# Performance work log

Hardware: AMD Instinct MI355X
Metric: run time of the kernel (lower is better)

The kernel has to match this reference:

```python
import jax, jax.numpy as jnp
import numpy as np
from jax import lax

B, T_ENC, T_DEC = 512, 64, 64
A = 64            # num_activities (pad token id = A)
ATTR_V = 10       # categorical attr vocab
ATTR_E, ACT_E, CF, ZD = 16, 64, 512, 128
TOT_ATTR = ATTR_E + 1           # 17
TDIM = TOT_ATTR // 2 + CF       # 8 + 512 = 520


def _lin(x, W, b):
    # torch nn.Linear: W is [out, in]
    return x @ W.T + b


def _cell(x, h, c, Wih, Whh, b):
    # torch LSTM cell, gate order i,f,g,o
    g = x @ Wih.T + h @ Whh.T + b
    i, f, gg, o = jnp.split(g, 4, axis=-1)
    c = jax.nn.sigmoid(f) * c + jax.nn.sigmoid(i) * jnp.tanh(gg)
    h = jax.nn.sigmoid(o) * jnp.tanh(c)
    return h, c


def setup_inputs() -> dict:
    key = jax.random.key(0)
    ks = iter(jax.random.split(key, 64))
    def n(shape, s=0.05):
        return jax.random.normal(next(ks), shape, jnp.float32) * s
    rng = np.random.default_rng(0)
    lens = rng.integers(2, T_ENC, size=B)
    acts_np = rng.integers(0, A - 1, size=(B, T_ENC))
    acts_np[np.arange(T_ENC)[None, :] >= lens[:, None]] = A  # pad token (max value -> argmax = len)
    return dict(
        attr_cat=jnp.asarray(rng.integers(0, ATTR_V, size=B), jnp.int32),
        attr_num=jax.random.uniform(next(ks), (B,), jnp.float32),
        acts=jnp.asarray(acts_np, jnp.int32),
        ts=jax.random.uniform(next(ks), (B, T_ENC), jnp.float32),
        epsilon=n((B, ZD), 1.0),
        attr_emb=n((ATTR_V, ATTR_E)),
        a2a_W=n((TOT_ATTR // 2, TOT_ATTR)), a2a_b=n((TOT_ATTR // 2,)),
        act_emb=n((A + 1, ACT_E)).at[A].set(0.0),  # padding_idx row zeroed
        eWih=n((4 * CF, ACT_E + 1)), eWhh=n((4 * CF, CF)), ebih=n((4 * CF,)), ebhh=n((4 * CF,)),
        mean_W=n((ZD, TDIM)), mean_b=n((ZD,)),
        var_W=n((ZD, TDIM)), var_b=n((ZD,)),
        z2t_W=n((TDIM, ZD)), z2t_b=n((TDIM,)),
        tc1_W=n((TDIM // 2, TDIM)), tc1_b=n((TDIM // 2,)),
        tc2_W=n((ATTR_V, TDIM // 2)), tc2_b=n((ATTR_V,)),
        tn1_W=n((TDIM // 2, TDIM)), tn1_b=n((TDIM // 2,)),
        tn2_W=n((1, TDIM // 2)), tn2_b=n((1,)),
        aWih=n((4 * CF, TDIM + ACT_E)), aWhh=n((4 * CF, CF)), abih=n((4 * CF,)), abhh=n((4 * CF,)),
        tWih=n((4 * CF, TDIM + ACT_E + 1)), tWhh=n((4 * CF, CF)), tbih=n((4 * CF,)), tbhh=n((4 * CF,)),
        e2act_W=n((A, CF)), e2act_b=n((A,)),
        ts1_W=n((CF // 2, CF)), ts1_b=n((CF // 2,)),
        ts2_W=n((1, CF // 2)), ts2_b=n((1,)),
    )


def reference(attr_cat, attr_num, acts, ts, epsilon,
              attr_emb, a2a_W, a2a_b, act_emb,
              eWih, eWhh, ebih, ebhh,
              mean_W, mean_b, var_W, var_b,
              z2t_W, z2t_b,
              tc1_W, tc1_b, tc2_W, tc2_b,
              tn1_W, tn1_b, tn2_W, tn2_b,
              aWih, aWhh, abih, abhh,
              tWih, tWhh, tbih, tbhh,
              e2act_W, e2act_b,
              ts1_W, ts1_b, ts2_W, ts2_b):
    # ---------- Encoder ----------
    e_attrs = jnp.concatenate([attr_emb[attr_cat], attr_num[:, None]], axis=1)   # [B,17]
    e_attrs = jax.nn.relu(_lin(e_attrs, a2a_W, a2a_b))                            # [B,8]
    x = jnp.concatenate([act_emb[acts], ts[:, :, None]], axis=2)                  # [B,T,ACT_E+1]
    eb = ebih + ebhh
    def enc_step(carry, xt):
        h, c = carry
        h, c = _cell(xt, h, c, eWih, eWhh, eb)
        return (h, c), h
    h0 = jnp.zeros((x.shape[0], CF), x.dtype)
    _, hs = lax.scan(enc_step, (h0, h0), jnp.swapaxes(x, 0, 1))
    cf_all = jnp.swapaxes(hs, 0, 1)                                               # [B,T,CF]
    # packed-sequence equivalence: LSTM is causal, we only read step lens-1
    lens = jnp.argmax(acts, axis=1)
    cf = cf_all[jnp.arange(cf_all.shape[0]), lens - 1]                            # [B,CF]
    t = jnp.concatenate([e_attrs, cf], axis=1)                                    # [B,TDIM]
    mean = _lin(t, mean_W, mean_b)
    var = _lin(t, var_W, var_b)
    z = mean + var * epsilon                                                      # reparameterization
    # ---------- Decoder ----------
    t_rec = jax.nn.relu(_lin(z, z2t_W, z2t_b))                                    # [B,TDIM]
    attr_cat_rec = jax.nn.softmax(_lin(jax.nn.relu(_lin(t_rec, tc1_W, tc1_b)), tc2_W, tc2_b), axis=1)
    attr_num_rec = jax.nn.sigmoid(_lin(jax.nn.relu(_lin(t_rec, tn1_W, tn1_b)), tn2_W, tn2_b))
    Bsz = t_rec.shape[0]
    ab, tb = abih + abhh, tbih + tbhh
    eot = jnp.broadcast_to(act_emb[A - 1], (Bsz, ACT_E))
    carry0 = (h0, h0, h0, h0, eot, jnp.zeros((Bsz, 1), t_rec.dtype))
    def dec_step(carry, _):
        h_a, c_a, h_t, c_t, ae, tsc = carry
        h_a, c_a = _cell(jnp.concatenate([t_rec, ae], 1), h_a, c_a, aWih, aWhh, ab)
        logits = _lin(h_a, e2act_W, e2act_b)                                      # [B,A]
        ae2 = act_emb[jnp.argmax(logits, axis=1)]                                 # greedy feedback
        h_t, c_t = _cell(jnp.concatenate([t_rec, ae2, tsc], 1), h_t, c_t, tWih, tWhh, tb)
        tsn = _lin(jax.nn.relu(_lin(h_t, ts1_W, ts1_b)), ts2_W, ts2_b)            # [B,1]
        return (h_a, c_a, h_t, c_t, ae2, tsn), (logits, tsn[:, 0])
    _, (logits_all, ts_all) = lax.scan(dec_step, carry0, None, length=T_DEC)
    acts_rec = jax.nn.softmax(jnp.swapaxes(logits_all, 0, 1), axis=2)             # [B,T_DEC,A]
    ts_rec = jnp.swapaxes(ts_all, 0, 1)                                           # [B,T_DEC]
    return (attr_cat_rec, attr_num_rec, acts_rec, ts_rec, mean, var)
```

## Files before the change

kernel.cpp:

```cpp
#include <hip/hip_runtime.h>
#include <math.h>


#define B 512
#define TT 64
#define CF 512
#define G4 2048
#define ZD 128
#define TDIM 520

typedef unsigned short u16;
typedef unsigned int u32;
typedef unsigned long long u64;
typedef short bf16x8 __attribute__((ext_vector_type(8)));
typedef float f32x4 __attribute__((ext_vector_type(4)));

__device__ __forceinline__ float sigm(float x) { return 1.f / (1.f + expf(-x)); }
__device__ __forceinline__ u16 f2bf(float f) {
    unsigned u = __float_as_uint(f);
    u += 0x7fffu + ((u >> 16) & 1u);
    return (u16)(u >> 16);
}
__device__ __forceinline__ float bf2f(u16 s) { return __uint_as_float(((unsigned)s) << 16); }
__device__ __forceinline__ u32 packbf(float v) {
    u16 hh = f2bf(v);
    u16 hl = f2bf(v - bf2f(hh));
    return (u32)hh | ((u32)hl << 16);
}

__device__ __forceinline__ void ast32(u32* p, u32 v) {
    __hip_atomic_store(p, v, __ATOMIC_RELAXED, __HIP_MEMORY_SCOPE_AGENT);
}
__device__ __forceinline__ u64 ald64(const u64* p) {
    return __hip_atomic_load(p, __ATOMIC_RELAXED, __HIP_MEMORY_SCOPE_AGENT);
}
__device__ __forceinline__ void astf(float* p, float v) {
    __hip_atomic_store(p, v, __ATOMIC_RELAXED, __HIP_MEMORY_SCOPE_AGENT);
}
__device__ __forceinline__ float aldf(const float* p) {
    return __hip_atomic_load(p, __ATOMIC_RELAXED, __HIP_MEMORY_SCOPE_AGENT);
}

__device__ __forceinline__ void unpk8(u64 a, u64 b, u64 c, u64 d,
                                      uint4& hi, uint4& lo) {
    u32 a0 = (u32)a, a1 = (u32)(a >> 32);
    u32 b0 = (u32)b, b1 = (u32)(b >> 32);
    u32 c0 = (u32)c, c1 = (u32)(c >> 32);
    u32 d0 = (u32)d, d1 = (u32)(d >> 32);
    hi.x = (a0 & 0xffffu) | (a1 << 16);  lo.x = (a0 >> 16) | (a1 & 0xffff0000u);
    hi.y = (b0 & 0xffffu) | (b1 << 16);  lo.y = (b0 >> 16) | (b1 & 0xffff0000u);
    hi.z = (c0 & 0xffffu) | (c1 << 16);  lo.z = (c0 >> 16) | (c1 & 0xffff0000u);
    hi.w = (d0 & 0xffffu) | (d1 << 16);  lo.w = (d0 >> 16) | (d1 & 0xffff0000u);
}

__device__ __forceinline__ void gsync_fast(int* bar, int target) {
    __syncthreads();
    if (threadIdx.x == 0) {
        __hip_atomic_fetch_add(bar, 1, __ATOMIC_RELEASE, __HIP_MEMORY_SCOPE_AGENT);
        while (__hip_atomic_load(bar, __ATOMIC_RELAXED, __HIP_MEMORY_SCOPE_AGENT) < target)
            __builtin_amdgcn_s_sleep(2);
    }
    __syncthreads();
}

__device__ __forceinline__ void gsync_full(int* bar, int target) {
    __syncthreads();
    if (threadIdx.x == 0) {
        __threadfence();
        __hip_atomic_fetch_add(bar, 1, __ATOMIC_ACQ_REL, __HIP_MEMORY_SCOPE_AGENT);
        while (__hip_atomic_load(bar, __ATOMIC_ACQUIRE, __HIP_MEMORY_SCOPE_AGENT) < target)
            __builtin_amdgcn_s_sleep(2);
        __threadfence();
    }
    __syncthreads();
}

struct __align__(16) GemmShared {
    u16 A[2][2][64][40];
    u16 Bw[2][2][64][40];
};

template<int TERMS>
__device__ __forceinline__ void gemm64i(
    GemmShared& sh,
    const u32* __restrict__ A32, int lda,
    const u16* __restrict__ Bh, const u16* __restrict__ Bl, int K,
    f32x4 acc[4])
{
    const int tid = threadIdx.x;
    const int lane = tid & 63, ws = tid >> 6;
    const int fr = lane & 15, quad = lane >> 4, ko = quad << 3;
    const int srr = tid >> 2, skq = (tid & 3) << 3;

    const u64* xp = (const u64*)(A32 + srr * lda + skq);
    const u16* wph = Bh + srr * K + skq;
    const u16* wpl = (TERMS == 3) ? (Bl + srr * K + skq) : (const u16*)0;

    const int niter = K >> 5;
    {
        u64 d0 = ald64(xp), d1 = ald64(xp + 1), d2 = ald64(xp + 2), d3 = ald64(xp + 3);
        uint4 hi, lo; unpk8(d0, d1, d2, d3, hi, lo);
        *(uint4*)&sh.A[0][0][srr][skq] = hi;
        *(uint4*)&sh.A[0][1][srr][skq] = lo;
        *(uint4*)&sh.Bw[0][0][srr][skq] = *(const uint4*)(wph);
        if (TERMS == 3) *(uint4*)&sh.Bw[0][1][srr][skq] = *(const uint4*)(wpl);
    }
    __syncthreads();

    for (int i = 0; i < niter; ++i) {
        const int cur = i & 1, nxt = cur ^ 1;
        u64 p0, p1, p2, p3; uint4 pbh, pbl;
        const bool pf = (i + 1 < niter);
        if (pf) {
            int k = (i + 1) << 5;
            const u64* xq = xp + (k >> 1);
            p0 = ald64(xq); p1 = ald64(xq + 1); p2 = ald64(xq + 2); p3 = ald64(xq + 3);
            pbh = *(const uint4*)(wph + k);
            if (TERMS == 3) pbl = *(const uint4*)(wpl + k);
        }
        bf16x8 ah = *(const bf16x8*)&sh.A[cur][0][(ws << 4) + fr][ko];
        bf16x8 al = *(const bf16x8*)&sh.A[cur][1][(ws << 4) + fr][ko];
        #pragma unroll
        for (int nt = 0; nt < 4; ++nt) {
            bf16x8 bh = *(const bf16x8*)&sh.Bw[cur][0][(nt << 4) + fr][ko];
            acc[nt] = __builtin_amdgcn_mfma_f32_16x16x32_bf16(ah, bh, acc[nt], 0, 0, 0);
            if (TERMS == 3) {
                bf16x8 bl = *(const bf16x8*)&sh.Bw[cur][1][(nt << 4) + fr][ko];
                acc[nt] = __builtin_amdgcn_mfma_f32_16x16x32_bf16(ah, bl, acc[nt], 0, 0, 0);
            }
            acc[nt] = __builtin_amdgcn_mfma_f32_16x16x32_bf16(al, bh, acc[nt], 0, 0, 0);
        }
        if (pf) {
            uint4 hi, lo; unpk8(p0, p1, p2, p3, hi, lo);
            *(uint4*)&sh.A[nxt][0][srr][skq] = hi;
            *(uint4*)&sh.A[nxt][1][srr][skq] = lo;
            *(uint4*)&sh.Bw[nxt][0][srr][skq] = pbh;
            if (TERMS == 3) *(uint4*)&sh.Bw[nxt][1][srr][skq] = pbl;
        }
        __syncthreads();
    }
}

__device__ __forceinline__ void ts_strip(
    GemmShared& sh, const u32* __restrict__ Xt32r,
    const u16* __restrict__ W1h, const float* __restrict__ b1,
    const float* __restrict__ w2, int ncg, float s[4])
{
    const int lane = threadIdx.x & 63;
    const int fr = lane & 15;
    f32x4 ac[4] = {};
    gemm64i<2>(sh, Xt32r, 512, W1h + (size_t)(ncg << 6) * 512, nullptr, 512, ac);
    s[0] = s[1] = s[2] = s[3] = 0.f;
    #pragma unroll
    for (int nt = 0; nt < 4; ++nt) {
        int j = (ncg << 6) + (nt << 4) + fr;
        float b1v = b1[j], w2v = w2[j];
        s[0] += fmaxf(ac[nt][0] + b1v, 0.f) * w2v;
        s[1] += fmaxf(ac[nt][1] + b1v, 0.f) * w2v;
        s[2] += fmaxf(ac[nt][2] + b1v, 0.f) * w2v;
        s[3] += fmaxf(ac[nt][3] + b1v, 0.f) * w2v;
    }
    #pragma unroll
    for (int off = 1; off < 16; off <<= 1) {
        s[0] += __shfl_xor(s[0], off);
        s[1] += __shfl_xor(s[1], off);
        s[2] += __shfl_xor(s[2], off);
        s[3] += __shfl_xor(s[3], off);
    }
}

__global__ __launch_bounds__(256, 1) void enc_coop(
    u32* __restrict__ Xe32,
    const u16* __restrict__ Weh, const u16* __restrict__ Wel,
    const float* __restrict__ biaspk,
    float* __restrict__ tcat, const int* __restrict__ lens,
    const int* __restrict__ acts, const float* __restrict__ tsv,
    const float* __restrict__ act_emb, int* __restrict__ bars)
{
    __shared__ GemmShared sh;
    const int bx = blockIdx.x, by = blockIdx.y, row0 = by << 6;
    const int tid = threadIdx.x, lane = tid & 63, ws = tid >> 6;
    const int fr = lane & 15, quad = lane >> 4;
    const int cell = (bx << 4) + fr;
    const int rbase = row0 + (ws << 4) + (quad << 2);
    int* bar = bars + by * 32;
    int gen = 0;

    float bb[4], ce[4] = {0.f, 0.f, 0.f, 0.f};
    int lm1[4];
    #pragma unroll
    for (int g = 0; g < 4; ++g) bb[g] = biaspk[(bx << 6) + (g << 4) + fr];
    #pragma unroll
    for (int r = 0; r < 4; ++r) lm1[r] = lens[rbase + r] - 1;

    for (int t = 0; t < TT; ++t) {
        const u32* xc = Xe32 + (size_t)(t & 1) * B * 608;
        u32* xn = Xe32 + (size_t)((t + 1) & 1) * B * 608;

        f32x4 acc[4] = {};
        gemm64i<3>(sh, xc + (size_t)row0 * 608, 608,
                   Weh + (size_t)(bx << 6) * 608, Wel + (size_t)(bx << 6) * 608, 608, acc);

        #pragma unroll
        for (int r = 0; r < 4; ++r) {
            int b = rbase + r;
            float gi = acc[0][r] + bb[0], gf = acc[1][r] + bb[1];
            float gg = acc[2][r] + bb[2], go = acc[3][r] + bb[3];
            float cn = sigm(gf) * ce[r] + sigm(gi) * tanhf(gg);
            ce[r] = cn;
            float h = sigm(go) * tanhf(cn);
            ast32(&xn[b * 608 + 65 + cell], packbf(h));
            if (t == lm1[r]) tcat[b * TDIM + 8 + cell] = h;
        }
        if (t < TT - 1) {
            for (int idx = tid; idx < 130; idx += 256) {
                int hi2 = (idx >= 65);
                int r = (bx << 1) + hi2, cc = idx - hi2 * 65;
                int b = row0 + r;
                float v = (cc < 64) ? act_emb[acts[(b << 6) + t + 1] * 64 + cc]
                                    : tsv[(b << 6) + t + 1];
                ast32(&xn[b * 608 + cc], packbf(v));
            }
            gsync_fast(bar, (++gen) * 32);
        }
    }
}

__global__ __launch_bounds__(256, 1) void dec_coop(
    u32* __restrict__ Xa32,
    u16* Wah, u16* Wal,
    const float* __restrict__ aWih, const float* __restrict__ aWhh,
    const float* __restrict__ base_a,
    u32* __restrict__ Xt32,
    const u16* __restrict__ Wth, const u16* __restrict__ Wtl,
    const float* __restrict__ base_t,
    const u16* __restrict__ E2h, const u16* __restrict__ E2l,
    const float* __restrict__ e2b, const float* __restrict__ act_emb,
    float* __restrict__ out_acts, float* __restrict__ out_ts,
    const u16* __restrict__ W1h, const float* __restrict__ b1,
    const float* __restrict__ w2, const float* __restrict__ b2p,
    float* __restrict__ tspart, int* __restrict__ bars)
{
    __shared__ GemmShared sh;
    __shared__ u16 ae2h[64][64];
    __shared__ u16 ae2l[64][64];
    const int bx = blockIdx.x, by = blockIdx.y, row0 = by << 6;
    const int tid = threadIdx.x, lane = tid & 63, ws = tid >> 6;
    const int fr = lane & 15, quad = lane >> 4;
    const int srr = tid >> 2, skq = (tid & 3) << 3;
    const bool bx0 = (bx == 0);
    const int cell = (bx << 4) + fr;
    const int rb0 = (ws << 4) + (quad << 2);
    const int rbase = row0 + rb0;
    const float tsb2 = b2p[0];
    int* barG = bars + 512;
    int* bar  = bars + 256 + by * 32;
    int gen = 0;

    {
        const int gtid = (((by << 5) + bx) << 8) + tid;
        for (int idx = gtid; idx < G4 * 576; idx += 32 * 8 * 256) {
            int np = idx / 576, k = idx - np * 576;
            int g = (np & 63) >> 4;
            int n = (g << 9) + (((np >> 6) << 4) + (np & 15));
            float v = (k < 64) ? aWih[n * 584 + 520 + k] : aWhh[(n << 9) + k - 64];
            u16 h = f2bf(v);
            Wah[idx] = h; Wal[idx] = f2bf(v - bf2f(h));
        }
    }

    float e2bv[4];
    float ca_r[4] = {0.f, 0.f, 0.f, 0.f}, ct_r[4] = {0.f, 0.f, 0.f, 0.f};
    #pragma unroll
    for (int nt = 0; nt < 4; ++nt) e2bv[nt] = e2b[(nt << 4) + fr];

    gsync_full(barG, 256);

    for (int t = 0; t < TT; ++t) {
        u32* xac = Xa32 + (size_t)(t & 1) * B * 576;
        u32* xan = Xa32 + (size_t)((t + 1) & 1) * B * 576;
        const u32* xtc = Xt32 + (size_t)(t & 1) * B * 512;
        u32* xtn = Xt32 + (size_t)((t + 1) & 1) * B * 512;

        {
            f32x4 acc[4] = {};
            gemm64i<3>(sh, xac + (size_t)row0 * 576, 576,
                       Wah + (size_t)(bx << 6) * 576, Wal + (size_t)(bx << 6) * 576, 576, acc);
            #pragma unroll
            for (int r = 0; r < 4; ++r) {
                int b = rbase + r;
                const float* bp = base_a + (size_t)b * G4 + (bx << 6) + fr;
                float gi = acc[0][r] + bp[0], gf = acc[1][r] + bp[16];
                float gg = acc[2][r] + bp[32], go = acc[3][r] + bp[48];
                float cn = sigm(gf) * ca_r[r] + sigm(gi) * tanhf(gg);
                ca_r[r] = cn;
                float h = sigm(go) * tanhf(cn);
                ast32(&xan[b * 576 + 64 + cell], packbf(h));
            }
            if (bx < 4 && t > 0) {
                float s[4];
                ts_strip(sh, xtc + (size_t)row0 * 512, W1h, b1, w2, bx, s);
                if (fr == 0) {
                    #pragma unroll
                    for (int r = 0; r < 4; ++r) astf(&tspart[(bx << 9) + rbase + r], s[r]);
                }
            }
        }
        gsync_fast(bar, (++gen) * 32);

        if (t > 0 && bx == 1 && tid < 64) {
            int b = row0 + tid;
            out_ts[(b << 6) + t - 1] =
                aldf(&tspart[b]) + aldf(&tspart[512 + b]) +
                aldf(&tspart[1024 + b]) + aldf(&tspart[1536 + b]) + tsb2;
        }
        {
            f32x4 acc[4] = {};
            gemm64i<3>(sh, xan + (size_t)row0 * 576 + 64, 576, E2h, E2l, 512, acc);
            #pragma unroll
            for (int r = 0; r < 4; ++r) {
                float l0 = acc[0][r] + e2bv[0], l1 = acc[1][r] + e2bv[1];
                float l2 = acc[2][r] + e2bv[2], l3 = acc[3][r] + e2bv[3];
                float m = fmaxf(fmaxf(l0, l1), fmaxf(l2, l3));
                #pragma unroll
                for (int off = 1; off < 16; off <<= 1) m = fmaxf(m, __shfl_xor(m, off));
                float e0 = expf(l0 - m), e1 = expf(l1 - m);
                float e2v = expf(l2 - m), e3 = expf(l3 - m);
                float sm = e0 + e1 + e2v + e3;
                #pragma unroll
                for (int off = 1; off < 16; off <<= 1) sm += __shfl_xor(sm, off);
                float bv = l0; int bc = fr;
                if (l1 > bv) { bv = l1; bc = 16 + fr; }
                if (l2 > bv) { bv = l2; bc = 32 + fr; }
                if (l3 > bv) { bv = l3; bc = 48 + fr; }
                #pragma unroll
                for (int off = 1; off < 16; off <<= 1) {
                    float ov = __shfl_xor(bv, off);
                    int oc = __shfl_xor(bc, off);
                    if (ov > bv || (ov == bv && oc < bc)) { bv = ov; bc = oc; }
                }
                int rl = rb0 + r, b = row0 + rl;
                if (bx0) {
                    float inv = 1.f / sm;
                    float* op = out_acts + (((size_t)(b << 6) + t) << 6);
                    op[fr] = e0 * inv; op[16 + fr] = e1 * inv;
                    op[32 + fr] = e2v * inv; op[48 + fr] = e3 * inv;
                }
                #pragma unroll
                for (int ci = 0; ci < 4; ++ci) {
                    int cc = (fr << 2) + ci;
                    float v = act_emb[(bc << 6) + cc];
                    u16 hh = f2bf(v), hl = f2bf(v - bf2f(hh));
                    ae2h[rl][cc] = hh; ae2l[rl][cc] = hl;
                    if (bx0) ast32(&xan[b * 576 + cc], ((u32)hh) | ((u32)hl << 16));
                }
            }
        }
        __syncthreads();

        f32x4 acc[4] = {};
        {
            const u32* Xt = xtc + (size_t)row0 * 512;
            const u16* wph = Wth + (size_t)((bx << 6) + srr) * 608 + skq;
            const u16* wpl = Wtl + (size_t)((bx << 6) + srr) * 608 + skq;
            const int ko = quad << 3;
            for (int i = 0; i < 19; ++i) {
                int k0 = i << 5;
                uint4 vh, vl;
                if (i < 16) {
                    const u64* p = (const u64*)(Xt + srr * 512 + k0 + skq);
                    u64 d0 = ald64(p), d1 = ald64(p + 1), d2 = ald64(p + 2), d3 = ald64(p + 3);
                    unpk8(d0, d1, d2, d3, vh, vl);
                } else if (i < 18) {
                    int co = k0 - 512 + skq;
                    vh = *(const uint4*)&ae2h[srr][co];
                    vl = *(const uint4*)&ae2l[srr][co];
                } else {
                    union U { uint4 q; u16 s[8]; } uh, ul;
                    uh.q = make_uint4(0, 0, 0, 0); ul.q = make_uint4(0, 0, 0, 0);
                    if (skq == 0) {
                        float ts = 0.f;
                        if (t > 0) {
                            int b = row0 + srr;
                            ts = aldf(&tspart[b]) + aldf(&tspart[512 + b]) +
                                 aldf(&tspart[1024 + b]) + aldf(&tspart[1536 + b]) + tsb2;
                        }
                        u16 hh = f2bf(ts);
                        uh.s[0] = hh; ul.s[0] = f2bf(ts - bf2f(hh));
                    }
                    vh = uh.q; vl = ul.q;
                }
                uint4 wh = *(const uint4*)(wph + k0);
                uint4 wl = *(const uint4*)(wpl + k0);
                __syncthreads();
                *(uint4*)&sh.A[0][0][srr][skq] = vh;
                *(uint4*)&sh.A[0][1][srr][skq] = vl;
                *(uint4*)&sh.Bw[0][0][srr][skq] = wh;
                *(uint4*)&sh.Bw[0][1][srr][skq] = wl;
                __syncthreads();
                bf16x8 ah = *(const bf16x8*)&sh.A[0][0][(ws << 4) + fr][ko];
                bf16x8 al = *(const bf16x8*)&sh.A[0][1][(ws << 4) + fr][ko];
                #pragma unroll
                for (int nt = 0; nt < 4; ++nt) {
                    bf16x8 bh = *(const bf16x8*)&sh.Bw[0][0][(nt << 4) + fr][ko];
                    bf16x8 bl = *(const bf16x8*)&sh.Bw[0][1][(nt << 4) + fr][ko];
                    acc[nt] = __builtin_amdgcn_mfma_f32_16x16x32_bf16(ah, bh, acc[nt], 0, 0, 0);
                    acc[nt] = __builtin_amdgcn_mfma_f32_16x16x32_bf16(ah, bl, acc[nt], 0, 0, 0);
                    acc[nt] = __builtin_amdgcn_mfma_f32_16x16x32_bf16(al, bh, acc[nt], 0, 0, 0);
                }
            }
        }
        #pragma unroll
        for (int r = 0; r < 4; ++r) {
            int b = rbase + r;
            const float* bp = base_t + (size_t)b * G4 + (bx << 6) + fr;
            float gi = acc[0][r] + bp[0], gf = acc[1][r] + bp[16];
            float gg = acc[2][r] + bp[32], go = acc[3][r] + bp[48];
            float cn = sigm(gf) * ct_r[r] + sigm(gi) * tanhf(gg);
            ct_r[r] = cn;
            float h = sigm(go) * tanhf(cn);
            ast32(&xtn[(b << 9) + cell], packbf(h));
        }
        gsync_fast(bar, (++gen) * 32);
    }

    if (bx < 4) {
        float s[4];
        ts_strip(sh, Xt32 + (size_t)row0 * 512, W1h, b1, w2, bx, s);
        if (fr == 0) {
            #pragma unroll
            for (int r = 0; r < 4; ++r) astf(&tspart[(bx << 9) + rbase + r], s[r]);
        }
    }
    gsync_fast(bar, (++gen) * 32);
    if (bx == 0 && tid < 64) {
        int b = row0 + tid;
        out_ts[(b << 6) + 63] =
            aldf(&tspart[b]) + aldf(&tspart[512 + b]) +
            aldf(&tspart[1024 + b]) + aldf(&tspart[1536 + b]) + tsb2;
    }
}

__device__ __forceinline__ int perm_src(int np) {
    int g = (np & 63) >> 4;
    int cell = ((np >> 6) << 4) + (np & 15);
    return (g << 9) + cell;
}

__global__ __launch_bounds__(256) void gemm_tn(
    const float* __restrict__ A, const float* __restrict__ Am,
    const float* __restrict__ Av, const float* __restrict__ Ae, int lda,
    const float* __restrict__ W1p, int ldw1,
    const float* __restrict__ W2p, int ldw2,
    int N, int K,
    const float* __restrict__ b1p, const float* __restrict__ b2p,
    float* __restrict__ C1, float* __restrict__ C2, int ldc,
    int relu, int permW)
{
    const float* W = W1p; int ldw = ldw1;
    const float* bias = b1p; float* C = C1;
    if (blockIdx.z == 1) { W = W2p; ldw = ldw2; bias = b2p; C = C2; }

    __shared__ __align__(16) float As[32][68];
    __shared__ __align__(16) float Ws[32][68];
    const int tid = threadIdx.x;
    const int tx = tid & 15, ty = tid >> 4;
    const int row0 = blockIdx.y << 6;
    const int col0 = blockIdx.x << 6;

    float acc[4][4] = {};

    for (int k0 = 0; k0 < K; k0 += 32) {
        #pragma unroll
        for (int s = 0; s < 2; ++s) {
            int f = tid + (s << 8);
            int rr = f >> 3;
            int kq = (f & 7) << 2;
            int k = k0 + kq;
            float4 v = make_float4(0.f, 0.f, 0.f, 0.f);
            size_t ro = (size_t)(row0 + rr) * (size_t)lda;
            if (Am) {
                if (k + 3 < K) {
                    float4 m = *(const float4*)(Am + ro + k);
                    float4 vv = *(const float4*)(Av + ro + k);
                    float4 e = *(const float4*)(Ae + ro + k);
                    v.x = fmaf(vv.x, e.x, m.x); v.y = fmaf(vv.y, e.y, m.y);
                    v.z = fmaf(vv.z, e.z, m.z); v.w = fmaf(vv.w, e.w, m.w);
                } else {
                    if (k + 0 < K) v.x = fmaf(Av[ro + k], Ae[ro + k], Am[ro + k]);
                    if (k + 1 < K) v.y = fmaf(Av[ro + k + 1], Ae[ro + k + 1], Am[ro + k + 1]);
                    if (k + 2 < K) v.z = fmaf(Av[ro + k + 2], Ae[ro + k + 2], Am[ro + k + 2]);
                }
            } else {
                const float* ap = A + ro;
                if (k + 3 < K) v = *(const float4*)(ap + k);
                else {
                    if (k + 0 < K) v.x = ap[k + 0];
                    if (k + 1 < K) v.y = ap[k + 1];
                    if (k + 2 < K) v.z = ap[k + 2];
                }
            }
            As[kq + 0][rr] = v.x; As[kq + 1][rr] = v.y;
            As[kq + 2][rr] = v.z; As[kq + 3][rr] = v.w;
        }
        #pragma unroll
        for (int s = 0; s < 2; ++s) {
            int f = tid + (s << 8);
            int rr = f >> 3;
            int kq = (f & 7) << 2;
            int k = k0 + kq;
            int n = col0 + rr;
            float4 v = make_float4(0.f, 0.f, 0.f, 0.f);
            if (n < N) {
                int nsrc = permW ? perm_src(n) : n;
                const float* wp = W + (size_t)nsrc * (size_t)ldw;
                if (k + 3 < K) v = *(const float4*)(wp + k);
                else {
                    if (k + 0 < K) v.x = wp[k + 0];
                    if (k + 1 < K) v.y = wp[k + 1];
                    if (k + 2 < K) v.z = wp[k + 2];
                }
            }
            Ws[kq + 0][rr] = v.x; Ws[kq + 1][rr] = v.y;
            Ws[kq + 2][rr] = v.z; Ws[kq + 3][rr] = v.w;
        }
        __syncthreads();
        #pragma unroll
        for (int k = 0; k < 32; ++k) {
            float4 av = *(const float4*)&As[k][ty << 2];
            float4 bv = *(const float4*)&Ws[k][tx << 2];
            acc[0][0] = fmaf(av.x, bv.x, acc[0][0]);
            acc[0][1] = fmaf(av.x, bv.y, acc[0][1]);
            acc[0][2] = fmaf(av.x, bv.z, acc[0][2]);
            acc[0][3] = fmaf(av.x, bv.w, acc[0][3]);
            acc[1][0] = fmaf(av.y, bv.x, acc[1][0]);
            acc[1][1] = fmaf(av.y, bv.y, acc[1][1]);
            acc[1][2] = fmaf(av.y, bv.z, acc[1][2]);
            acc[1][3] = fmaf(av.y, bv.w, acc[1][3]);
            acc[2][0] = fmaf(av.z, bv.x, acc[2][0]);
            acc[2][1] = fmaf(av.z, bv.y, acc[2][1]);
            acc[2][2] = fmaf(av.z, bv.z, acc[2][2]);
            acc[2][3] = fmaf(av.z, bv.w, acc[2][3]);
            acc[3][0] = fmaf(av.w, bv.x, acc[3][0]);
            acc[3][1] = fmaf(av.w, bv.y, acc[3][1]);
            acc[3][2] = fmaf(av.w, bv.z, acc[3][2]);
            acc[3][3] = fmaf(av.w, bv.w, acc[3][3]);
        }
        __syncthreads();
    }

    #pragma unroll
    for (int i = 0; i < 4; ++i) {
        int rr = row0 + (ty << 2) + i;
        float* cp = C + (size_t)rr * (size_t)ldc;
        #pragma unroll
        for (int j = 0; j < 4; ++j) {
            int cc = col0 + (tx << 2) + j;
            if (cc < N) {
                float v = acc[i][j];
                if (bias) v += bias[cc];
                if (relu) v = fmaxf(v, 0.f);
                cp[cc] = v;
            }
        }
    }
}

#define N_WE (G4 * 608)
#define N_WT (G4 * 608)
#define N_W1 (256 * 512)
#define N_E2 (64 * 512)
__global__ void pack_all(
    u16* __restrict__ Weh, u16* __restrict__ Wel,
    u16* __restrict__ Wth, u16* __restrict__ Wtl,
    u16* __restrict__ W1h,
    u16* __restrict__ E2h, u16* __restrict__ E2l,
    float* __restrict__ be, float* __restrict__ ba, float* __restrict__ bt,
    const float* __restrict__ eWih, const float* __restrict__ eWhh,
    const float* __restrict__ tWih, const float* __restrict__ tWhh,
    const float* __restrict__ ts1W, const float* __restrict__ e2W,
    const float* __restrict__ ebih, const float* __restrict__ ebhh,
    const float* __restrict__ abih, const float* __restrict__ abhh,
    const float* __restrict__ tbih, const float* __restrict__ tbhh)
{
    int idx = blockIdx.x * 256 + threadIdx.x;
    if (idx < N_WE) {
        int np = idx / 608, k = idx - np * 608;
        int n = perm_src(np);
        float v = 0.f;
        if (k < 65) v = eWih[n * 65 + k];
        else if (k < 577) v = eWhh[(n << 9) + k - 65];
        u16 h = f2bf(v); Weh[idx] = h; Wel[idx] = f2bf(v - bf2f(h));
        return;
    }
    idx -= N_WE;
    if (idx < N_WT) {
        int np = idx / 608, k = idx - np * 608;
        int n = perm_src(np);
        float v = 0.f;
        if (k < 512) v = tWhh[(n << 9) + k];
        else if (k < 576) v = tWih[n * 585 + 520 + (k - 512)];
        else if (k == 576) v = tWih[n * 585 + 584];
        u16 h = f2bf(v); Wth[idx] = h; Wtl[idx] = f2bf(v - bf2f(h));
        return;
    }
    idx -= N_WT;
    if (idx < N_W1) {
        W1h[idx] = f2bf(ts1W[idx]);
        return;
    }
    idx -= N_W1;
    if (idx < N_E2) {
        float v = e2W[idx];
        u16 h = f2bf(v); E2h[idx] = h; E2l[idx] = f2bf(v - bf2f(h));
        return;
    }
    idx -= N_E2;
    if (idx < G4) {
        int n = perm_src(idx);
        be[idx] = ebih[n] + ebhh[n];
        ba[idx] = abih[n] + abhh[n];
        bt[idx] = tbih[n] + tbhh[n];
    }
}

__global__ __launch_bounds__(256) void init_all(
    u32* __restrict__ xe0, u32* __restrict__ xe1,
    int* __restrict__ lens, float* __restrict__ tcat,
    u32* __restrict__ xa0, u32* __restrict__ xt0,
    const int* __restrict__ acts, const float* __restrict__ tsv,
    const float* __restrict__ act_emb,
    const int* __restrict__ attr_cat, const float* __restrict__ attr_num,
    const float* __restrict__ attr_emb,
    const float* __restrict__ a2aW, const float* __restrict__ a2ab,
    int* __restrict__ bars)
{
    int b = blockIdx.x, tid = threadIdx.x;
    if (b == 0) {
        for (int j = tid; j < 1024; j += 256)
            __hip_atomic_store(&bars[j], 0, __ATOMIC_RELAXED, __HIP_MEMORY_SCOPE_AGENT);
    }
    for (int j = tid; j < 608; j += 256) {
        float v = 0.f;
        if (j < 64) v = act_emb[acts[b << 6] * 64 + j];
        else if (j == 64) v = tsv[b << 6];
        xe0[b * 608 + j] = packbf(v);
        if (j >= 577) xe1[b * 608 + j] = 0;
    }
    for (int j = tid; j < CF; j += 256) {
        xt0[(b << 9) + j] = 0;
    }
    for (int j = tid; j < 576; j += 256) {
        float v = (j < 64) ? act_emb[63 * 64 + j] : 0.f;
        xa0[b * 576 + j] = packbf(v);
    }
    if (tid < 64) {
        int v = acts[(b << 6) + tid];
        int m = v;
        #pragma unroll
        for (int off = 32; off; off >>= 1) m = max(m, __shfl_xor(m, off));
        unsigned long long mask = __ballot(v == m);
        if (tid == 0) lens[b] = __ffsll(mask) - 1;
    }
    if (tid < 8) {
        const float* wr = a2aW + tid * 17;
        const float* em = attr_emb + attr_cat[b] * 16;
        float s = a2ab[tid];
        #pragma unroll
        for (int k = 0; k < 16; ++k) s = fmaf(em[k], wr[k], s);
        s = fmaf(attr_num[b], wr[16], s);
        tcat[b * TDIM + tid] = fmaxf(s, 0.f);
    }
}

__global__ __launch_bounds__(64) void attr_heads(
    const float* __restrict__ hid1, const float* __restrict__ hid2,
    const float* __restrict__ tc2W, const float* __restrict__ tc2b,
    const float* __restrict__ tn2W, const float* __restrict__ tn2b,
    float* __restrict__ out_cat, float* __restrict__ out_num) {
    __shared__ __align__(16) float h1[260], h2[260], sl[10];
    int b = blockIdx.x, tid = threadIdx.x;
    for (int k = tid; k < 260; k += 64) {
        h1[k] = hid1[b * 260 + k];
        h2[k] = hid2[b * 260 + k];
    }
    __syncthreads();
    if (tid < 10) {
        float l = tc2b[tid];
        const float* wr = tc2W + tid * 260;
        for (int k = 0; k < 260; ++k) l = fmaf(h1[k], wr[k], l);
        sl[tid] = l;
    }
    __syncthreads();
    if (tid < 10) {
        float m = sl[0];
        for (int i = 1; i < 10; ++i) m = fmaxf(m, sl[i]);
        float ssum = 0.f;
        for (int i = 0; i < 10; ++i) ssum += expf(sl[i] - m);
        out_cat[b * 10 + tid] = expf(sl[tid] - m) / ssum;
    }
    float p = 0.f;
    for (int k = tid; k < 260; k += 64) p = fmaf(h2[k], tn2W[k], p);
    #pragma unroll
    for (int off = 32; off; off >>= 1) p += __shfl_xor(p, off);
    if (tid == 0) out_num[b] = 1.f / (1.f + expf(-(p + tn2b[0])));
}

extern "C" void kernel_launch(void* const* d_in, const int* in_sizes, int n_in,
                              void* d_out, int out_size, void* d_ws, size_t ws_size,
                              hipStream_t stream) {
    const int*   attr_cat = (const int*)  d_in[0];
    const float* attr_num = (const float*)d_in[1];
    const int*   acts     = (const int*)  d_in[2];
    const float* tsv      = (const float*)d_in[3];
    const float* eps      = (const float*)d_in[4];
    const float* attr_emb = (const float*)d_in[5];
    const float* a2a_W    = (const float*)d_in[6];
    const float* a2a_b    = (const float*)d_in[7];
    const float* act_emb  = (const float*)d_in[8];
    const float* eWih     = (const float*)d_in[9];
    const float* eWhh     = (const float*)d_in[10];
    const float* ebih     = (const float*)d_in[11];
    const float* ebhh     = (const float*)d_in[12];
    const float* mean_W   = (const float*)d_in[13];
    const float* mean_b   = (const float*)d_in[14];
    const float* var_W    = (const float*)d_in[15];
    const float* var_b    = (const float*)d_in[16];
    const float* z2t_W    = (const float*)d_in[17];
    const float* z2t_b    = (const float*)d_in[18];
    const float* tc1_W    = (const float*)d_in[19];
    const float* tc1_b    = (const float*)d_in[20];
// ... 98 lines not shown
```

Measured before the change: 5.628 ms.

## Load MFMA operands directly from global memory, dropping LDS staging in GEMMs

Replaces the LDS double-buffered 64x64 GEMM tile with per-wave direct global loads of the A and B fragments into registers, removing the __syncthreads barriers and shared-memory round trips inside the recurrent step GEMMs. The time-decoder inner loop likewise drops its per-iteration LDS staging and hoists the timestamp feedback load out of the K loop, and the ae2 LDS arrays are padded. The trade is that each wave now reads B weights itself, so the same weight rows are fetched four times per block through L1/L2 with less coalesced access, and load latency is no longer hidden by the explicit double buffer.

```diff
diff --git a/kernel.cpp b/kernel.cpp
--- a/kernel.cpp
+++ b/kernel.cpp
@@ -52,6 +52,9 @@
     hi.z = (c0 & 0xffffu) | (c1 << 16);  lo.z = (c0 >> 16) | (c1 & 0xffff0000u);
     hi.w = (d0 & 0xffffu) | (d1 << 16);  lo.w = (d0 >> 16) | (d1 & 0xffff0000u);
 }
+__device__ __forceinline__ bf16x8 u4bf(uint4 v) {
+    union { uint4 u; bf16x8 b; } c; c.u = v; return c.b;
+}
 
 __device__ __forceinline__ void gsync_fast(int* bar, int target) {
     __syncthreads();
@@ -75,81 +78,51 @@
     __syncthreads();
 }
 
-struct __align__(16) GemmShared {
-    u16 A[2][2][64][40];
-    u16 Bw[2][2][64][40];
-};
-
 template<int TERMS>
-__device__ __forceinline__ void gemm64i(
-    GemmShared& sh,
+__device__ __forceinline__ void gemm64r(
     const u32* __restrict__ A32, int lda,
     const u16* __restrict__ Bh, const u16* __restrict__ Bl, int K,
     f32x4 acc[4])
 {
     const int tid = threadIdx.x;
-    const int lane = tid & 63, ws = tid >> 6;
-    const int fr = lane & 15, quad = lane >> 4, ko = quad << 3;
-    const int srr = tid >> 2, skq = (tid & 3) << 3;
-
-    const u64* xp = (const u64*)(A32 + srr * lda + skq);
-    const u16* wph = Bh + srr * K + skq;
-    const u16* wpl = (TERMS == 3) ? (Bl + srr * K + skq) : (const u16*)0;
-
+    const int lane = tid & 63;
+    const int ws = tid >> 6, fr = lane & 15, quad = lane >> 4, ko = quad << 3;
+    const int arow = (ws << 4) + fr;
+    const u64* ap = (const u64*)(A32 + arow * lda + ko);
+    const u16* bp0 = Bh + (size_t)fr * K + ko;
+    const u16* bl0 = (TERMS == 3) ? (Bl + (size_t)fr * K + ko) : (const u16*)0;
     const int niter = K >> 5;
-    {
-        u64 d0 = ald64(xp), d1 = ald64(xp + 1), d2 = ald64(xp + 2), d3 = ald64(xp + 3);
+    #pragma unroll 2
+    for (int i = 0; i < niter; ++i) {
+        const int k0 = i << 5;
+        u64 d0 = ald64(ap + (k0 >> 1));
+        u64 d1 = ald64(ap + (k0 >> 1) + 1);
+        u64 d2 = ald64(ap + (k0 >> 1) + 2);
+        u64 d3 = ald64(ap + (k0 >> 1) + 3);
         uint4 hi, lo; unpk8(d0, d1, d2, d3, hi, lo);
-        *(uint4*)&sh.A[0][0][srr][skq] = hi;
-        *(uint4*)&sh.A[0][1][srr][skq] = lo;
-        *(uint4*)&sh.Bw[0][0][srr][skq] = *(const uint4*)(wph);
-        if (TERMS == 3) *(uint4*)&sh.Bw[0][1][srr][skq] = *(const uint4*)(wpl);
-    }
-    __syncthreads();
-
-    for (int i = 0; i < niter; ++i) {
-        const int cur = i & 1, nxt = cur ^ 1;
-        u64 p0, p1, p2, p3; uint4 pbh, pbl;
-        const bool pf = (i + 1 < niter);
-        if (pf) {
-            int k = (i + 1) << 5;
-            const u64* xq = xp + (k >> 1);
-            p0 = ald64(xq); p1 = ald64(xq + 1); p2 = ald64(xq + 2); p3 = ald64(xq + 3);
-            pbh = *(const uint4*)(wph + k);
-            if (TERMS == 3) pbl = *(const uint4*)(wpl + k);
-        }
-        bf16x8 ah = *(const bf16x8*)&sh.A[cur][0][(ws << 4) + fr][ko];
-        bf16x8 al = *(const bf16x8*)&sh.A[cur][1][(ws << 4) + fr][ko];
+        bf16x8 ah = u4bf(hi), al = u4bf(lo);
         #pragma unroll
         for (int nt = 0; nt < 4; ++nt) {
-            bf16x8 bh = *(const bf16x8*)&sh.Bw[cur][0][(nt << 4) + fr][ko];
+            bf16x8 bh = *(const bf16x8*)(bp0 + (size_t)(nt << 4) * K + k0);
             acc[nt] = __builtin_amdgcn_mfma_f32_16x16x32_bf16(ah, bh, acc[nt], 0, 0, 0);
             if (TERMS == 3) {
-                bf16x8 bl = *(const bf16x8*)&sh.Bw[cur][1][(nt << 4) + fr][ko];
+                bf16x8 bl = *(const bf16x8*)(bl0 + (size_t)(nt << 4) * K + k0);
                 acc[nt] = __builtin_amdgcn_mfma_f32_16x16x32_bf16(ah, bl, acc[nt], 0, 0, 0);
             }
             acc[nt] = __builtin_amdgcn_mfma_f32_16x16x32_bf16(al, bh, acc[nt], 0, 0, 0);
         }
-        if (pf) {
-            uint4 hi, lo; unpk8(p0, p1, p2, p3, hi, lo);
-            *(uint4*)&sh.A[nxt][0][srr][skq] = hi;
-            *(uint4*)&sh.A[nxt][1][srr][skq] = lo;
-            *(uint4*)&sh.Bw[nxt][0][srr][skq] = pbh;
-            if (TERMS == 3) *(uint4*)&sh.Bw[nxt][1][srr][skq] = pbl;
-        }
-        __syncthreads();
     }
 }
 
 __device__ __forceinline__ void ts_strip(
-    GemmShared& sh, const u32* __restrict__ Xt32r,
+    const u32* __restrict__ Xt32r,
     const u16* __restrict__ W1h, const float* __restrict__ b1,
     const float* __restrict__ w2, int ncg, float s[4])
 {
     const int lane = threadIdx.x & 63;
     const int fr = lane & 15;
     f32x4 ac[4] = {};
-    gemm64i<2>(sh, Xt32r, 512, W1h + (size_t)(ncg << 6) * 512, nullptr, 512, ac);
+    gemm64r<2>(Xt32r, 512, W1h + (size_t)(ncg << 6) * 512, nullptr, 512, ac);
     s[0] = s[1] = s[2] = s[3] = 0.f;
     #pragma unroll
     for (int nt = 0; nt < 4; ++nt) {
@@ -177,7 +150,6 @@
     const int* __restrict__ acts, const float* __restrict__ tsv,
     const float* __restrict__ act_emb, int* __restrict__ bars)
 {
-    __shared__ GemmShared sh;
     const int bx = blockIdx.x, by = blockIdx.y, row0 = by << 6;
     const int tid = threadIdx.x, lane = tid & 63, ws = tid >> 6;
     const int fr = lane & 15, quad = lane >> 4;
@@ -198,7 +170,7 @@
         u32* xn = Xe32 + (size_t)((t + 1) & 1) * B * 608;
 
         f32x4 acc[4] = {};
-        gemm64i<3>(sh, xc + (size_t)row0 * 608, 608,
+        gemm64r<3>(xc + (size_t)row0 * 608, 608,
                    Weh + (size_t)(bx << 6) * 608, Wel + (size_t)(bx << 6) * 608, 608, acc);
 
         #pragma unroll
@@ -241,17 +213,16 @@
     const float* __restrict__ w2, const float* __restrict__ b2p,
     float* __restrict__ tspart, int* __restrict__ bars)
 {
-    __shared__ GemmShared sh;
-    __shared__ u16 ae2h[64][64];
-    __shared__ u16 ae2l[64][64];
+    __shared__ u16 ae2h[64][72];
+    __shared__ u16 ae2l[64][72];
     const int bx = blockIdx.x, by = blockIdx.y, row0 = by << 6;
     const int tid = threadIdx.x, lane = tid & 63, ws = tid >> 6;
     const int fr = lane & 15, quad = lane >> 4;
-    const int srr = tid >> 2, skq = (tid & 3) << 3;
     const bool bx0 = (bx == 0);
     const int cell = (bx << 4) + fr;
     const int rb0 = (ws << 4) + (quad << 2);
     const int rbase = row0 + rb0;
+    const int arow = (ws << 4) + fr;
     const float tsb2 = b2p[0];
     int* barG = bars + 512;
     int* bar  = bars + 256 + by * 32;
@@ -284,7 +255,7 @@
 
         {
             f32x4 acc[4] = {};
-            gemm64i<3>(sh, xac + (size_t)row0 * 576, 576,
+            gemm64r<3>(xac + (size_t)row0 * 576, 576,
                        Wah + (size_t)(bx << 6) * 576, Wal + (size_t)(bx << 6) * 576, 576, acc);
             #pragma unroll
             for (int r = 0; r < 4; ++r) {
@@ -299,7 +270,7 @@
             }
             if (bx < 4 && t > 0) {
                 float s[4];
-                ts_strip(sh, xtc + (size_t)row0 * 512, W1h, b1, w2, bx, s);
+                ts_strip(xtc + (size_t)row0 * 512, W1h, b1, w2, bx, s);
                 if (fr == 0) {
                     #pragma unroll
                     for (int r = 0; r < 4; ++r) astf(&tspart[(bx << 9) + rbase + r], s[r]);
@@ -316,7 +287,7 @@
         }
         {
             f32x4 acc[4] = {};
-            gemm64i<3>(sh, xan + (size_t)row0 * 576 + 64, 576, E2h, E2l, 512, acc);
+            gemm64r<3>(xan + (size_t)row0 * 576 + 64, 576, E2h, E2l, 512, acc);
             #pragma unroll
             for (int r = 0; r < 4; ++r) {
                 float l0 = acc[0][r] + e2bv[0], l1 = acc[1][r] + e2bv[1];
@@ -360,50 +331,45 @@
 
         f32x4 acc[4] = {};
         {
-            const u32* Xt = xtc + (size_t)row0 * 512;
-            const u16* wph = Wth + (size_t)((bx << 6) + srr) * 608 + skq;
-            const u16* wpl = Wtl + (size_t)((bx << 6) + srr) * 608 + skq;
             const int ko = quad << 3;
+            const u64* ap = (const u64*)(xtc + (size_t)row0 * 512 + arow * 512 + ko);
+            const u16* bp0h = Wth + (size_t)((bx << 6) + fr) * 608 + ko;
+            const u16* bp0l = Wtl + (size_t)((bx << 6) + fr) * 608 + ko;
+            float tsq = 0.f;
+            if (t > 0) {
+                int b = row0 + arow;
+                tsq = aldf(&tspart[b]) + aldf(&tspart[512 + b]) +
+                      aldf(&tspart[1024 + b]) + aldf(&tspart[1536 + b]) + tsb2;
+            }
+            #pragma unroll 2
             for (int i = 0; i < 19; ++i) {
-                int k0 = i << 5;
-                uint4 vh, vl;
+                const int k0 = i << 5;
+                bf16x8 ah, al;
                 if (i < 16) {
-                    const u64* p = (const u64*)(Xt + srr * 512 + k0 + skq);
-                    u64 d0 = ald64(p), d1 = ald64(p + 1), d2 = ald64(p + 2), d3 = ald64(p + 3);
-                    unpk8(d0, d1, d2, d3, vh, vl);
+                    u64 d0 = ald64(ap + (k0 >> 1));
+                    u64 d1 = ald64(ap + (k0 >> 1) + 1);
+                    u64 d2 = ald64(ap + (k0 >> 1) + 2);
+                    u64 d3 = ald64(ap + (k0 >> 1) + 3);
+                    uint4 hi, lo; unpk8(d0, d1, d2, d3, hi, lo);
+                    ah = u4bf(hi); al = u4bf(lo);
                 } else if (i < 18) {
-                    int co = k0 - 512 + skq;
-                    vh = *(const uint4*)&ae2h[srr][co];
-                    vl = *(const uint4*)&ae2l[srr][co];
+                    int co = k0 - 512 + ko;
+                    ah = *(const bf16x8*)&ae2h[arow][co];
+                    al = *(const bf16x8*)&ae2l[arow][co];
                 } else {
-                    union U { uint4 q; u16 s[8]; } uh, ul;
-                    uh.q = make_uint4(0, 0, 0, 0); ul.q = make_uint4(0, 0, 0, 0);
-                    if (skq == 0) {
-                        float ts = 0.f;
-                        if (t > 0) {
-                            int b = row0 + srr;
-                            ts = aldf(&tspart[b]) + aldf(&tspart[512 + b]) +
-                                 aldf(&tspart[1024 + b]) + aldf(&tspart[1536 + b]) + tsb2;
-                        }
-                        u16 hh = f2bf(ts);
-                        uh.s[0] = hh; ul.s[0] = f2bf(ts - bf2f(hh));
+                    union { uint4 u; bf16x8 b; } zh, zl;
+                    zh.u = make_uint4(0, 0, 0, 0); zl.u = make_uint4(0, 0, 0, 0);
+                    if (quad == 0) {
+                        u16 hh = f2bf(tsq);
+                        zh.u.x = (u32)hh;
+                        zl.u.x = (u32)f2bf(tsq - bf2f(hh));
                     }
-                    vh = uh.q; vl = ul.q;
-                }
-                uint4 wh = *(const uint4*)(wph + k0);
-                uint4 wl = *(const uint4*)(wpl + k0);
-                __syncthreads();
-                *(uint4*)&sh.A[0][0][srr][skq] = vh;
-                *(uint4*)&sh.A[0][1][srr][skq] = vl;
-                *(uint4*)&sh.Bw[0][0][srr][skq] = wh;
-                *(uint4*)&sh.Bw[0][1][srr][skq] = wl;
-                __syncthreads();
-                bf16x8 ah = *(const bf16x8*)&sh.A[0][0][(ws << 4) + fr][ko];
-                bf16x8 al = *(const bf16x8*)&sh.A[0][1][(ws << 4) + fr][ko];
+                    ah = zh.b; al = zl.b;
+                }
                 #pragma unroll
                 for (int nt = 0; nt < 4; ++nt) {
-                    bf16x8 bh = *(const bf16x8*)&sh.Bw[0][0][(nt << 4) + fr][ko];
-                    bf16x8 bl = *(const bf16x8*)&sh.Bw[0][1][(nt << 4) + fr][ko];
+                    bf16x8 bh = *(const bf16x8*)(bp0h + (size_t)(nt << 4) * 608 + k0);
+                    bf16x8 bl = *(const bf16x8*)(bp0l + (size_t)(nt << 4) * 608 + k0);
                     acc[nt] = __builtin_amdgcn_mfma_f32_16x16x32_bf16(ah, bh, acc[nt], 0, 0, 0);
                     acc[nt] = __builtin_amdgcn_mfma_f32_16x16x32_bf16(ah, bl, acc[nt], 0, 0, 0);
                     acc[nt] = __builtin_amdgcn_mfma_f32_16x16x32_bf16(al, bh, acc[nt], 0, 0, 0);
@@ -426,7 +392,7 @@
 
     if (bx < 4) {
         float s[4];
-        ts_strip(sh, Xt32 + (size_t)row0 * 512, W1h, b1, w2, bx, s);
+        ts_strip(Xt32 + (size_t)row0 * 512, W1h, b1, w2, bx, s);
         if (fr == 0) {
             #pragma unroll
             for (int r = 0; r < 4; ++r) astf(&tspart[(bx << 9) + rbase + r], s[r]);
```

New measurement: 10.36 ms. +84.1%, slower.

## Deepen GEMM prefetch pipeline and route decoder t-cell GEMM through it

Applied to the files above, without the earlier changes.

Restructures the shared gemm64i helper to keep two register prefetch stages in flight (loads for iteration i+2 issued ahead) with explicit ping-pong shared buffers, so global-load latency is hidden better in every recurrent step. The decoder t-cell's first 16 K-chunks now use this pipelined helper via a new ldb stride parameter, instead of a serial single-buffer loop with two barriers per chunk. The tspart reduction is hoisted out of that loop, and the ae2 shared arrays are padded to cut LDS bank conflicts. The extra prefetch stage raises register pressure, which could hurt at launch_bounds(256,1).

```diff
diff --git a/kernel.cpp b/kernel.cpp
--- a/kernel.cpp
+++ b/kernel.cpp
@@ -80,21 +80,62 @@
     u16 Bw[2][2][64][40];
 };
 
+struct Pref { u64 a0, a1, a2, a3; uint4 bh, bl; };
+
+template<int TERMS>
+__device__ __forceinline__ void pf_issue(Pref& p, const u64* xp,
+        const u16* wph, const u16* wpl, int it) {
+    const int k = it << 5;
+    const u64* xq = xp + (k >> 1);
+    p.a0 = ald64(xq); p.a1 = ald64(xq + 1);
+    p.a2 = ald64(xq + 2); p.a3 = ald64(xq + 3);
+    p.bh = *(const uint4*)(wph + k);
+    if (TERMS == 3) p.bl = *(const uint4*)(wpl + k);
+}
+
+template<int TERMS>
+__device__ __forceinline__ void pf_write(GemmShared& sh, const Pref& p,
+        int nxt, int srr, int skq) {
+    uint4 hi, lo; unpk8(p.a0, p.a1, p.a2, p.a3, hi, lo);
+    *(uint4*)&sh.A[nxt][0][srr][skq] = hi;
+    *(uint4*)&sh.A[nxt][1][srr][skq] = lo;
+    *(uint4*)&sh.Bw[nxt][0][srr][skq] = p.bh;
+    if (TERMS == 3) *(uint4*)&sh.Bw[nxt][1][srr][skq] = p.bl;
+}
+
+template<int TERMS>
+__device__ __forceinline__ void pf_comp(GemmShared& sh, int cur,
+        int row, int ko, int fr, f32x4 acc[4]) {
+    bf16x8 ah = *(const bf16x8*)&sh.A[cur][0][row][ko];
+    bf16x8 al = *(const bf16x8*)&sh.A[cur][1][row][ko];
+    #pragma unroll
+    for (int nt = 0; nt < 4; ++nt) {
+        bf16x8 bh = *(const bf16x8*)&sh.Bw[cur][0][(nt << 4) + fr][ko];
+        acc[nt] = __builtin_amdgcn_mfma_f32_16x16x32_bf16(ah, bh, acc[nt], 0, 0, 0);
+        if (TERMS == 3) {
+            bf16x8 bl = *(const bf16x8*)&sh.Bw[cur][1][(nt << 4) + fr][ko];
+            acc[nt] = __builtin_amdgcn_mfma_f32_16x16x32_bf16(ah, bl, acc[nt], 0, 0, 0);
+        }
+        acc[nt] = __builtin_amdgcn_mfma_f32_16x16x32_bf16(al, bh, acc[nt], 0, 0, 0);
+    }
+}
+
 template<int TERMS>
 __device__ __forceinline__ void gemm64i(
     GemmShared& sh,
     const u32* __restrict__ A32, int lda,
-    const u16* __restrict__ Bh, const u16* __restrict__ Bl, int K,
+    const u16* __restrict__ Bh, const u16* __restrict__ Bl, int K, int ldb,
     f32x4 acc[4])
 {
     const int tid = threadIdx.x;
     const int lane = tid & 63, ws = tid >> 6;
     const int fr = lane & 15, quad = lane >> 4, ko = quad << 3;
     const int srr = tid >> 2, skq = (tid & 3) << 3;
+    const int row = (ws << 4) + fr;
 
     const u64* xp = (const u64*)(A32 + srr * lda + skq);
-    const u16* wph = Bh + srr * K + skq;
-    const u16* wpl = (TERMS == 3) ? (Bl + srr * K + skq) : (const u16*)0;
+    const u16* wph = Bh + srr * ldb + skq;
+    const u16* wpl = (TERMS == 3) ? (Bl + srr * ldb + skq) : (const u16*)0;
 
     const int niter = K >> 5;
     {
@@ -105,39 +146,27 @@
         *(uint4*)&sh.Bw[0][0][srr][skq] = *(const uint4*)(wph);
         if (TERMS == 3) *(uint4*)&sh.Bw[0][1][srr][skq] = *(const uint4*)(wpl);
     }
+    Pref pA, pB;
+    if (niter > 1) pf_issue<TERMS>(pA, xp, wph, wpl, 1);
+    if (niter > 2) pf_issue<TERMS>(pB, xp, wph, wpl, 2);
     __syncthreads();
 
-    for (int i = 0; i < niter; ++i) {
-        const int cur = i & 1, nxt = cur ^ 1;
-        u64 p0, p1, p2, p3; uint4 pbh, pbl;
-        const bool pf = (i + 1 < niter);
-        if (pf) {
-            int k = (i + 1) << 5;
-            const u64* xq = xp + (k >> 1);
-            p0 = ald64(xq); p1 = ald64(xq + 1); p2 = ald64(xq + 2); p3 = ald64(xq + 3);
-            pbh = *(const uint4*)(wph + k);
-            if (TERMS == 3) pbl = *(const uint4*)(wpl + k);
-        }
-        bf16x8 ah = *(const bf16x8*)&sh.A[cur][0][(ws << 4) + fr][ko];
-        bf16x8 al = *(const bf16x8*)&sh.A[cur][1][(ws << 4) + fr][ko];
-        #pragma unroll
-        for (int nt = 0; nt < 4; ++nt) {
-            bf16x8 bh = *(const bf16x8*)&sh.Bw[cur][0][(nt << 4) + fr][ko];
-            acc[nt] = __builtin_amdgcn_mfma_f32_16x16x32_bf16(ah, bh, acc[nt], 0, 0, 0);
-            if (TERMS == 3) {
-                bf16x8 bl = *(const bf16x8*)&sh.Bw[cur][1][(nt << 4) + fr][ko];
-                acc[nt] = __builtin_amdgcn_mfma_f32_16x16x32_bf16(ah, bl, acc[nt], 0, 0, 0);
-            }
-            acc[nt] = __builtin_amdgcn_mfma_f32_16x16x32_bf16(al, bh, acc[nt], 0, 0, 0);
-        }
-        if (pf) {
-            uint4 hi, lo; unpk8(p0, p1, p2, p3, hi, lo);
-            *(uint4*)&sh.A[nxt][0][srr][skq] = hi;
-            *(uint4*)&sh.A[nxt][1][srr][skq] = lo;
-            *(uint4*)&sh.Bw[nxt][0][srr][skq] = pbh;
-            if (TERMS == 3) *(uint4*)&sh.Bw[nxt][1][srr][skq] = pbl;
+    int i = 0;
+    for (;;) {
+        pf_comp<TERMS>(sh, 0, row, ko, fr, acc);
+        if (i + 1 < niter) {
+            pf_write<TERMS>(sh, pA, 1, srr, skq);
+            if (i + 3 < niter) pf_issue<TERMS>(pA, xp, wph, wpl, i + 3);
         }
         __syncthreads();
+        if (++i >= niter) break;
+        pf_comp<TERMS>(sh, 1, row, ko, fr, acc);
+        if (i + 1 < niter) {
+            pf_write<TERMS>(sh, pB, 0, srr, skq);
+            if (i + 3 < niter) pf_issue<TERMS>(pB, xp, wph, wpl, i + 3);
+        }
+        __syncthreads();
+        if (++i >= niter) break;
     }
 }
 
@@ -149,7 +178,7 @@
     const int lane = threadIdx.x & 63;
     const int fr = lane & 15;
     f32x4 ac[4] = {};
-    gemm64i<2>(sh, Xt32r, 512, W1h + (size_t)(ncg << 6) * 512, nullptr, 512, ac);
+    gemm64i<2>(sh, Xt32r, 512, W1h + (size_t)(ncg << 6) * 512, nullptr, 512, 512, ac);
     s[0] = s[1] = s[2] = s[3] = 0.f;
     #pragma unroll
     for (int nt = 0; nt < 4; ++nt) {
@@ -199,7 +228,8 @@
 
         f32x4 acc[4] = {};
         gemm64i<3>(sh, xc + (size_t)row0 * 608, 608,
-                   Weh + (size_t)(bx << 6) * 608, Wel + (size_t)(bx << 6) * 608, 608, acc);
+                   Weh + (size_t)(bx << 6) * 608, Wel + (size_t)(bx << 6) * 608,
+                   608, 608, acc);
 
         #pragma unroll
         for (int r = 0; r < 4; ++r) {
@@ -242,8 +272,8 @@
     float* __restrict__ tspart, int* __restrict__ bars)
 {
     __shared__ GemmShared sh;
-    __shared__ u16 ae2h[64][64];
-    __shared__ u16 ae2l[64][64];
+    __shared__ u16 ae2h[64][72];
+    __shared__ u16 ae2l[64][72];
     const int bx = blockIdx.x, by = blockIdx.y, row0 = by << 6;
     const int tid = threadIdx.x, lane = tid & 63, ws = tid >> 6;
     const int fr = lane & 15, quad = lane >> 4;
@@ -285,7 +315,8 @@
         {
             f32x4 acc[4] = {};
             gemm64i<3>(sh, xac + (size_t)row0 * 576, 576,
-                       Wah + (size_t)(bx << 6) * 576, Wal + (size_t)(bx << 6) * 576, 576, acc);
+                       Wah + (size_t)(bx << 6) * 576, Wal + (size_t)(bx << 6) * 576,
+                       576, 576, acc);
             #pragma unroll
             for (int r = 0; r < 4; ++r) {
                 int b = rbase + r;
@@ -314,9 +345,15 @@
                 aldf(&tspart[b]) + aldf(&tspart[512 + b]) +
                 aldf(&tspart[1024 + b]) + aldf(&tspart[1536 + b]) + tsb2;
         }
+        float tsq = 0.f;
+        if (t > 0) {
+            int b = row0 + srr;
+            tsq = aldf(&tspart[b]) + aldf(&tspart[512 + b]) +
+                  aldf(&tspart[1024 + b]) + aldf(&tspart[1536 + b]) + tsb2;
+        }
         {
             f32x4 acc[4] = {};
-            gemm64i<3>(sh, xan + (size_t)row0 * 576 + 64, 576, E2h, E2l, 512, acc);
+            gemm64i<3>(sh, xan + (size_t)row0 * 576 + 64, 576, E2h, E2l, 512, 512, acc);
             #pragma unroll
             for (int r = 0; r < 4; ++r) {
                 float l0 = acc[0][r] + e2bv[0], l1 = acc[1][r] + e2bv[1];
@@ -359,19 +396,17 @@
         __syncthreads();
 
         f32x4 acc[4] = {};
+        gemm64i<3>(sh, xtc + (size_t)row0 * 512, 512,
+                   Wth + (size_t)(bx << 6) * 608, Wtl + (size_t)(bx << 6) * 608,
+                   512, 608, acc);
         {
-            const u32* Xt = xtc + (size_t)row0 * 512;
             const u16* wph = Wth + (size_t)((bx << 6) + srr) * 608 + skq;
             const u16* wpl = Wtl + (size_t)((bx << 6) + srr) * 608 + skq;
             const int ko = quad << 3;
-            for (int i = 0; i < 19; ++i) {
+            for (int i = 16; i < 19; ++i) {
                 int k0 = i << 5;
                 uint4 vh, vl;
-                if (i < 16) {
-                    const u64* p = (const u64*)(Xt + srr * 512 + k0 + skq);
-                    u64 d0 = ald64(p), d1 = ald64(p + 1), d2 = ald64(p + 2), d3 = ald64(p + 3);
-                    unpk8(d0, d1, d2, d3, vh, vl);
-                } else if (i < 18) {
+                if (i < 18) {
                     int co = k0 - 512 + skq;
                     vh = *(const uint4*)&ae2h[srr][co];
                     vl = *(const uint4*)&ae2l[srr][co];
@@ -379,14 +414,8 @@
                     union U { uint4 q; u16 s[8]; } uh, ul;
                     uh.q = make_uint4(0, 0, 0, 0); ul.q = make_uint4(0, 0, 0, 0);
                     if (skq == 0) {
-                        float ts = 0.f;
-                        if (t > 0) {
-                            int b = row0 + srr;
-                            ts = aldf(&tspart[b]) + aldf(&tspart[512 + b]) +
-                                 aldf(&tspart[1024 + b]) + aldf(&tspart[1536 + b]) + tsb2;
-                        }
-                        u16 hh = f2bf(ts);
-                        uh.s[0] = hh; ul.s[0] = f2bf(ts - bf2f(hh));
+                        u16 hh = f2bf(tsq);
+                        uh.s[0] = hh; ul.s[0] = f2bf(tsq - bf2f(hh));
                     }
                     vh = uh.q; vl = ul.q;
                 }
```

New measurement: 4.904 ms. 1.15x faster.
